# Performance work log

Measured on AMD Instinct MI355X. Metric: run time of the kernel, lower is better.

## Reference

```python
import jax, jax.numpy as jnp
import numpy as np

EPS = 1e-6
MOMENTUM = 0.9


def _normalize(x, eps=EPS):
    # Matches torch F.normalize: x / clamp_min(||x||, eps)
    n = jnp.linalg.norm(x, axis=-1, keepdims=True)
    return x / jnp.maximum(n, eps)


def setup_inputs() -> dict:
    key = jax.random.key(0)
    k1, k2 = jax.random.split(key)
    embeddings = jax.random.normal(k1, (131072, 512), dtype=jnp.float32)
    prototypes = jax.random.normal(k2, (1024, 512), dtype=jnp.float32)
    return {"embeddings": embeddings, "prototypes": prototypes}


def reference(embeddings, prototypes):
    # Steady-state update path of PrototypeBank.update (filled == bank_size).
    K = prototypes.shape[0]
    e = _normalize(embeddings)                      # [N, D]
    active = _normalize(prototypes)                 # [K, D]
    sims = jnp.einsum('nd,kd->nk', e, active)       # [N, K]
    assign = jnp.argmax(sims, axis=1)               # [N] int
    # per-prototype masked mean via segment reduction
    sums = jax.ops.segment_sum(e, assign, num_segments=K)          # [K, D]
    counts = jax.ops.segment_sum(jnp.ones((e.shape[0],), e.dtype), assign,
                                 num_segments=K)                    # [K]
    has = counts > 0
    cluster_mean = sums / jnp.maximum(counts, 1.0)[:, None]
    # EMA uses the RAW stored prototype (not the normalized copy), then renormalizes
    updated = MOMENTUM * prototypes + (1.0 - MOMENTUM) * cluster_mean
    updated = _normalize(updated)
    new_prototypes = jnp.where(has[:, None], updated, prototypes)
    return new_prototypes
```

## Files before the change

kernel.cpp:

```cpp
#include <hip/hip_runtime.h>


#define D 512
#define NPROTO 1024
#define ROWS 64

typedef __attribute__((ext_vector_type(8))) unsigned short ushort8;
typedef __attribute__((ext_vector_type(8))) __bf16 bfrag8;
typedef __attribute__((ext_vector_type(4))) float f32x4;

static __device__ inline unsigned short f2bf(float f) {
    unsigned int u = __float_as_uint(f);
    u = u + 0x7FFFu + ((u >> 16) & 1u);
    return (unsigned short)(u >> 16);
}

__global__ __launch_bounds__(256) void norm_protos_kernel(
    const float* __restrict__ protos, unsigned short* __restrict__ pbf,
    int* __restrict__ counts)
{
    const int wave = threadIdx.x >> 6, lane = threadIdx.x & 63;
    const int row = blockIdx.x * 4 + wave;
    const float* src = protos + (size_t)row * D + lane * 8;
    float4 v0 = *(const float4*)src;
    float4 v1 = *(const float4*)(src + 4);
    float ss = v0.x*v0.x + v0.y*v0.y + v0.z*v0.z + v0.w*v0.w
             + v1.x*v1.x + v1.y*v1.y + v1.z*v1.z + v1.w*v1.w;
    #pragma unroll
    for (int off = 32; off > 0; off >>= 1) ss += __shfl_xor(ss, off, 64);
    const float inv = 1.0f / fmaxf(sqrtf(ss), 1e-6f);
    ushort8 w;
    w[0] = f2bf(v0.x*inv); w[1] = f2bf(v0.y*inv); w[2] = f2bf(v0.z*inv); w[3] = f2bf(v0.w*inv);
    w[4] = f2bf(v1.x*inv); w[5] = f2bf(v1.y*inv); w[6] = f2bf(v1.z*inv); w[7] = f2bf(v1.w*inv);
    const int g = row >> 4, cl = row & 15;
    const int ks = lane >> 2, q = lane & 3;
    *(ushort8*)(pbf + (size_t)(g * 16 + ks) * 512 + (q * 16 + cl) * 8) = w;
    if (blockIdx.x == 0) ((int4*)counts)[threadIdx.x] = (int4){0, 0, 0, 0};
}

__global__ __launch_bounds__(512, 4) void assign_kernel(
    const float* __restrict__ emb, const unsigned short* __restrict__ pbf,
    int* __restrict__ assign, float* __restrict__ invnorm, int* __restrict__ counts)
{
    __shared__ __align__(16) unsigned short eT[ROWS * D];
    const int tid = threadIdx.x;
    const int wave = tid >> 6, lane = tid & 63;
    const int rowbase = blockIdx.x * ROWS;
    const int cl = lane & 15, quad = lane >> 4;

    for (int rr = 0; rr < 8; ++rr) {
        const int rloc = wave * 8 + rr;
        const float* src = emb + (size_t)(rowbase + rloc) * D + lane * 8;
        float4 v0 = *(const float4*)src;
        float4 v1 = *(const float4*)(src + 4);
        float ss = v0.x*v0.x + v0.y*v0.y + v0.z*v0.z + v0.w*v0.w
                 + v1.x*v1.x + v1.y*v1.y + v1.z*v1.z + v1.w*v1.w;
        #pragma unroll
        for (int off = 32; off > 0; off >>= 1) ss += __shfl_xor(ss, off, 64);
        const float inv = 1.0f / fmaxf(sqrtf(ss), 1e-6f);
        if (lane == 0) invnorm[rowbase + rloc] = inv;
        ushort8 w;
        w[0] = f2bf(v0.x*inv); w[1] = f2bf(v0.y*inv); w[2] = f2bf(v0.z*inv); w[3] = f2bf(v0.w*inv);
        w[4] = f2bf(v1.x*inv); w[5] = f2bf(v1.y*inv); w[6] = f2bf(v1.z*inv); w[7] = f2bf(v1.w*inv);
        const int slot = lane ^ (rloc & 7);
        *(ushort8*)(&eT[rloc * D + slot * 8]) = w;
    }
    __syncthreads();

    float rmax[4][4];
    int   ridx[4][4];
    #pragma unroll
    for (int m = 0; m < 4; ++m)
        #pragma unroll
        for (int r = 0; r < 4; ++r) { rmax[m][r] = -3.4e38f; ridx[m][r] = 0; }

    const int colq = wave * 128;
    const unsigned short* bb = pbf + (size_t)colq * 512 + lane * 8;

    for (int ng = 0; ng < 2; ++ng) {
        const int colbase = colq + ng * 64;
        const unsigned short* bg = bb + (size_t)ng * 64 * 512;
        f32x4 acc[4][4];
        #pragma unroll
        for (int m = 0; m < 4; ++m)
            #pragma unroll
            for (int n = 0; n < 4; ++n) acc[m][n] = (f32x4){0.f, 0.f, 0.f, 0.f};

        #pragma unroll 2
        for (int ks = 0; ks < 16; ++ks) {
            bfrag8 a[4], b[4];
            #pragma unroll
            for (int m = 0; m < 4; ++m) {
                const int rloc = m * 16 + cl;
                const int slot = (ks * 4 + quad) ^ (rloc & 7);
                a[m] = *(const bfrag8*)(&eT[rloc * D + slot * 8]);
            }
            #pragma unroll
            for (int n = 0; n < 4; ++n)
                b[n] = *(const bfrag8*)(bg + n * 8192 + ks * 512);
            #pragma unroll
            for (int n = 0; n < 4; ++n)
                #pragma unroll
                for (int m = 0; m < 4; ++m)
                    acc[m][n] = __builtin_amdgcn_mfma_f32_16x16x32_bf16(a[m], b[n], acc[m][n], 0, 0, 0);
        }
        #pragma unroll
        for (int n = 0; n < 4; ++n) {
            const int idx = colbase + n * 16 + cl;
            #pragma unroll
            for (int m = 0; m < 4; ++m)
                #pragma unroll
                for (int r = 0; r < 4; ++r) {
                    const float v = acc[m][n][r];
                    if (v > rmax[m][r]) { rmax[m][r] = v; ridx[m][r] = idx; }
                }
        }
    }

    #pragma unroll
    for (int m = 0; m < 4; ++m)
        #pragma unroll
        for (int r = 0; r < 4; ++r) {
            float v = rmax[m][r]; int idx = ridx[m][r];
            #pragma unroll
            for (int off = 1; off < 16; off <<= 1) {
                const float ov = __shfl_xor(v, off, 64);
                const int   oi = __shfl_xor(idx, off, 64);
                if (ov > v || (ov == v && oi < idx)) { v = ov; idx = oi; }
            }
            rmax[m][r] = v; ridx[m][r] = idx;
        }

    __syncthreads();
    float* swmax = (float*)eT;
    int*   swidx = (int*)&eT[1024];
    if (cl == 0) {
        #pragma unroll
        for (int m = 0; m < 4; ++m)
            #pragma unroll
            for (int r = 0; r < 4; ++r) {
                const int lrow = m * 16 + quad * 4 + r;
                swmax[wave * 64 + lrow] = rmax[m][r];
                swidx[wave * 64 + lrow] = ridx[m][r];
            }
    }
    __syncthreads();
    if (tid < 64) {
        float v = swmax[tid]; int idx = swidx[tid];
        #pragma unroll
        for (int w = 1; w < 8; ++w) {
            const float ov = swmax[w * 64 + tid];
            const int   oi = swidx[w * 64 + tid];
            if (ov > v || (ov == v && oi < idx)) { v = ov; idx = oi; }
        }
        assign[rowbase + tid] = idx;
        atomicAdd(&counts[idx], 1);
    }
}

__global__ __launch_bounds__(1024) void prefix_kernel(
    const int* __restrict__ counts, int* __restrict__ offsets, int* __restrict__ cursor)
{
    __shared__ int sc[NPROTO];
    const int t = threadIdx.x;
    const int c = counts[t];
    sc[t] = c;
    __syncthreads();
    #pragma unroll
    for (int off = 1; off < NPROTO; off <<= 1) {
        const int v = (t >= off) ? sc[t - off] : 0;
        __syncthreads();
        sc[t] += v;
        __syncthreads();
    }
    const int excl = sc[t] - c;
    offsets[t] = excl;
    cursor[t]  = excl;
}

__global__ __launch_bounds__(256) void scatter_kernel(
    const int* __restrict__ assign, int* __restrict__ cursor, int* __restrict__ bin)
{
    const int i = blockIdx.x * 256 + threadIdx.x;
    const int k = assign[i];
    const int pos = atomicAdd(&cursor[k], 1);
    bin[pos] = i;
}

__global__ __launch_bounds__(256) void update_kernel(
    const float* __restrict__ emb, const float* __restrict__ protos,
    const int* __restrict__ bin, const int* __restrict__ counts,
    const int* __restrict__ offsets, const float* __restrict__ invnorm,
    float* __restrict__ out)
{
    __shared__ float red[4];
    const int k = blockIdx.x, t = threadIdx.x;
    const int cnt = counts[k], off = offsets[k];
    float acc0 = 0.f, acc1 = 0.f;

    int j = 0;
    for (; j + 4 <= cnt; j += 4) {
        const int r0 = bin[off + j],     r1 = bin[off + j + 1];
        const int r2 = bin[off + j + 2], r3 = bin[off + j + 3];
        const float s0 = invnorm[r0], s1 = invnorm[r1];
        const float s2 = invnorm[r2], s3 = invnorm[r3];
        const float2 v0 = *(const float2*)(emb + (size_t)r0 * D + 2 * t);
        const float2 v1 = *(const float2*)(emb + (size_t)r1 * D + 2 * t);
        const float2 v2 = *(const float2*)(emb + (size_t)r2 * D + 2 * t);
        const float2 v3 = *(const float2*)(emb + (size_t)r3 * D + 2 * t);
        acc0 += v0.x * s0; acc1 += v0.y * s0;
        acc0 += v1.x * s1; acc1 += v1.y * s1;
        acc0 += v2.x * s2; acc1 += v2.y * s2;
        acc0 += v3.x * s3; acc1 += v3.y * s3;
    }
    for (; j < cnt; ++j) {
        const int r = bin[off + j];
        const float s = invnorm[r];
        const float2 v = *(const float2*)(emb + (size_t)r * D + 2 * t);
        acc0 += v.x * s; acc1 += v.y * s;
    }

    const float denom = fmaxf((float)cnt, 1.0f);
    const float m0 = acc0 / denom, m1 = acc1 / denom;
    const float p0 = protos[(size_t)k * D + 2 * t];
    const float p1 = protos[(size_t)k * D + 2 * t + 1];
    const float u0 = 0.9f * p0 + 0.1f * m0;
    const float u1 = 0.9f * p1 + 0.1f * m1;
    float ss = u0 * u0 + u1 * u1;
    #pragma unroll
    for (int off2 = 32; off2 > 0; off2 >>= 1) ss += __shfl_xor(ss, off2, 64);
    if ((t & 63) == 0) red[t >> 6] = ss;
    __syncthreads();
    const float tot = red[0] + red[1] + red[2] + red[3];
    const float inv = 1.0f / fmaxf(sqrtf(tot), 1e-6f);
    out[(size_t)k * D + 2 * t]     = (cnt > 0) ? u0 * inv : p0;
    out[(size_t)k * D + 2 * t + 1] = (cnt > 0) ? u1 * inv : p1;
}

extern "C" void kernel_launch(void* const* d_in, const int* in_sizes, int n_in,
                              void* d_out, int out_size, void* d_ws, size_t ws_size,
                              hipStream_t stream)
{
    const float* emb    = (const float*)d_in[0];
    const float* protos = (const float*)d_in[1];
    float* out = (float*)d_out;
    const int n_emb = in_sizes[0] / D;

    char* ws = (char*)d_ws;
    unsigned short* pbf = (unsigned short*)ws;
    int*   assign  = (int*)  (ws + (1 << 20));
    float* invnorm = (float*)(ws + (1 << 20) + (512 << 10));
    int*   counts  = (int*)  (ws + (2 << 20));
    int*   offsets = (int*)  (ws + (2 << 20) + (4 << 10));
    int*   cursor  = (int*)  (ws + (2 << 20) + (8 << 10));
    int*   bin     = (int*)  (ws + (2 << 20) + (12 << 10));

    norm_protos_kernel<<<NPROTO / 4, 256, 0, stream>>>(protos, pbf, counts);
    assign_kernel<<<n_emb / ROWS, 512, 0, stream>>>(emb, pbf, assign, invnorm, counts);
    prefix_kernel<<<1, 1024, 0, stream>>>(counts, offsets, cursor);
    scatter_kernel<<<n_emb / 256, 256, 0, stream>>>(assign, cursor, bin);
    update_kernel<<<NPROTO, 256, 0, stream>>>(emb, protos, bin, counts, offsets, invnorm, out);
}
```

Before: 617.1 us.

## Drop per-row scaling before argmax, reduce argmax per tile, vectorize update gather

```diff
diff --git a/kernel.cpp b/kernel.cpp
--- a/kernel.cpp
+++ b/kernel.cpp
@@ -43,6 +43,8 @@
     int* __restrict__ assign, float* __restrict__ invnorm, int* __restrict__ counts)
 {
     __shared__ __align__(16) unsigned short eT[ROWS * D];
+    __shared__ float swmax[16][64];
+    __shared__ int   swidx[16][64];
     const int tid = threadIdx.x;
     const int wave = tid >> 6, lane = tid & 63;
     const int rowbase = blockIdx.x * ROWS;
@@ -57,42 +59,30 @@
                  + v1.x*v1.x + v1.y*v1.y + v1.z*v1.z + v1.w*v1.w;
         #pragma unroll
         for (int off = 32; off > 0; off >>= 1) ss += __shfl_xor(ss, off, 64);
-        const float inv = 1.0f / fmaxf(sqrtf(ss), 1e-6f);
-        if (lane == 0) invnorm[rowbase + rloc] = inv;
+        if (lane == 0) invnorm[rowbase + rloc] = 1.0f / fmaxf(sqrtf(ss), 1e-6f);
         ushort8 w;
-        w[0] = f2bf(v0.x*inv); w[1] = f2bf(v0.y*inv); w[2] = f2bf(v0.z*inv); w[3] = f2bf(v0.w*inv);
-        w[4] = f2bf(v1.x*inv); w[5] = f2bf(v1.y*inv); w[6] = f2bf(v1.z*inv); w[7] = f2bf(v1.w*inv);
+        w[0] = f2bf(v0.x); w[1] = f2bf(v0.y); w[2] = f2bf(v0.z); w[3] = f2bf(v0.w);
+        w[4] = f2bf(v1.x); w[5] = f2bf(v1.y); w[6] = f2bf(v1.z); w[7] = f2bf(v1.w);
         const int slot = lane ^ (rloc & 7);
         *(ushort8*)(&eT[rloc * D + slot * 8]) = w;
     }
     __syncthreads();
 
-    float rmax[4][4];
-    int   ridx[4][4];
-    #pragma unroll
-    for (int m = 0; m < 4; ++m)
-        #pragma unroll
-        for (int r = 0; r < 4; ++r) { rmax[m][r] = -3.4e38f; ridx[m][r] = 0; }
-
-    const int colq = wave * 128;
-    const unsigned short* bb = pbf + (size_t)colq * 512 + lane * 8;
-
     for (int ng = 0; ng < 2; ++ng) {
-        const int colbase = colq + ng * 64;
-        const unsigned short* bg = bb + (size_t)ng * 64 * 512;
+        const int colbase = wave * 128 + ng * 64;
+        const unsigned short* bg = pbf + (size_t)colbase * 512 + lane * 8;
         f32x4 acc[4][4];
         #pragma unroll
         for (int m = 0; m < 4; ++m)
             #pragma unroll
             for (int n = 0; n < 4; ++n) acc[m][n] = (f32x4){0.f, 0.f, 0.f, 0.f};
 
-        #pragma unroll 2
         for (int ks = 0; ks < 16; ++ks) {
             bfrag8 a[4], b[4];
             #pragma unroll
             for (int m = 0; m < 4; ++m) {
                 const int rloc = m * 16 + cl;
-                const int slot = (ks * 4 + quad) ^ (rloc & 7);
+                const int slot = (ks * 4 + quad) ^ (cl & 7);
                 a[m] = *(const bfrag8*)(&eT[rloc * D + slot * 8]);
             }
             #pragma unroll
@@ -104,53 +94,39 @@
                 for (int m = 0; m < 4; ++m)
                     acc[m][n] = __builtin_amdgcn_mfma_f32_16x16x32_bf16(a[m], b[n], acc[m][n], 0, 0, 0);
         }
-        #pragma unroll
-        for (int n = 0; n < 4; ++n) {
-            const int idx = colbase + n * 16 + cl;
-            #pragma unroll
-            for (int m = 0; m < 4; ++m)
+
+        #pragma unroll
+        for (int m = 0; m < 4; ++m)
+            #pragma unroll
+            for (int r = 0; r < 4; ++r) {
+                float v = acc[m][0][r];
+                int idx = colbase + cl;
                 #pragma unroll
-                for (int r = 0; r < 4; ++r) {
-                    const float v = acc[m][n][r];
-                    if (v > rmax[m][r]) { rmax[m][r] = v; ridx[m][r] = idx; }
+                for (int n = 1; n < 4; ++n) {
+                    const float c = acc[m][n][r];
+                    const int ci = colbase + n * 16 + cl;
+                    if (c > v) { v = c; idx = ci; }
                 }
-        }
-    }
-
-    #pragma unroll
-    for (int m = 0; m < 4; ++m)
-        #pragma unroll
-        for (int r = 0; r < 4; ++r) {
-            float v = rmax[m][r]; int idx = ridx[m][r];
-            #pragma unroll
-            for (int off = 1; off < 16; off <<= 1) {
-                const float ov = __shfl_xor(v, off, 64);
-                const int   oi = __shfl_xor(idx, off, 64);
-                if (ov > v || (ov == v && oi < idx)) { v = ov; idx = oi; }
+                #pragma unroll
+                for (int off = 1; off < 16; off <<= 1) {
+                    const float ov = __shfl_xor(v, off, 64);
+                    const int   oi = __shfl_xor(idx, off, 64);
+                    if (ov > v || (ov == v && oi < idx)) { v = ov; idx = oi; }
+                }
+                if (cl == 0) {
+                    swmax[wave * 2 + ng][m * 16 + quad * 4 + r] = v;
+                    swidx[wave * 2 + ng][m * 16 + quad * 4 + r] = idx;
+                }
             }
-            rmax[m][r] = v; ridx[m][r] = idx;
-        }
-
-    __syncthreads();
-    float* swmax = (float*)eT;
-    int*   swidx = (int*)&eT[1024];
-    if (cl == 0) {
-        #pragma unroll
-        for (int m = 0; m < 4; ++m)
-            #pragma unroll
-            for (int r = 0; r < 4; ++r) {
-                const int lrow = m * 16 + quad * 4 + r;
-                swmax[wave * 64 + lrow] = rmax[m][r];
-                swidx[wave * 64 + lrow] = ridx[m][r];
-            }
-    }
-    __syncthreads();
+    }
+    __syncthreads();
+
     if (tid < 64) {
-        float v = swmax[tid]; int idx = swidx[tid];
-        #pragma unroll
-        for (int w = 1; w < 8; ++w) {
-            const float ov = swmax[w * 64 + tid];
-            const int   oi = swidx[w * 64 + tid];
+        float v = swmax[0][tid]; int idx = swidx[0][tid];
+        #pragma unroll
+        for (int s = 1; s < 16; ++s) {
+            const float ov = swmax[s][tid];
+            const int   oi = swidx[s][tid];
             if (ov > v || (ov == v && oi < idx)) { v = ov; idx = oi; }
         }
         assign[rowbase + tid] = idx;
@@ -193,48 +169,67 @@
     const int* __restrict__ offsets, const float* __restrict__ invnorm,
     float* __restrict__ out)
 {
-    __shared__ float red[4];
+    __shared__ float4 part[128];
+    __shared__ float red[2];
     const int k = blockIdx.x, t = threadIdx.x;
     const int cnt = counts[k], off = offsets[k];
-    float acc0 = 0.f, acc1 = 0.f;
-
-    int j = 0;
-    for (; j + 4 <= cnt; j += 4) {
-        const int r0 = bin[off + j],     r1 = bin[off + j + 1];
-        const int r2 = bin[off + j + 2], r3 = bin[off + j + 3];
+    const int par = t >> 7, colg = (t & 127) * 4;
+    float4 acc = make_float4(0.f, 0.f, 0.f, 0.f);
+
+    int jb = 0;
+    for (; jb + 4 <= cnt; jb += 4) {
+        const int r0 = bin[off + jb + par];
+        const int r1 = bin[off + jb + 2 + par];
         const float s0 = invnorm[r0], s1 = invnorm[r1];
-        const float s2 = invnorm[r2], s3 = invnorm[r3];
-        const float2 v0 = *(const float2*)(emb + (size_t)r0 * D + 2 * t);
-        const float2 v1 = *(const float2*)(emb + (size_t)r1 * D + 2 * t);
-        const float2 v2 = *(const float2*)(emb + (size_t)r2 * D + 2 * t);
-        const float2 v3 = *(const float2*)(emb + (size_t)r3 * D + 2 * t);
-        acc0 += v0.x * s0; acc1 += v0.y * s0;
-        acc0 += v1.x * s1; acc1 += v1.y * s1;
-        acc0 += v2.x * s2; acc1 += v2.y * s2;
-        acc0 += v3.x * s3; acc1 += v3.y * s3;
-    }
-    for (; j < cnt; ++j) {
-        const int r = bin[off + j];
+        const float4 v0 = *(const float4*)(emb + (size_t)r0 * D + colg);
+        const float4 v1 = *(const float4*)(emb + (size_t)r1 * D + colg);
+        acc.x += v0.x * s0; acc.y += v0.y * s0; acc.z += v0.z * s0; acc.w += v0.w * s0;
+        acc.x += v1.x * s1; acc.y += v1.y * s1; acc.z += v1.z * s1; acc.w += v1.w * s1;
+    }
+    if (jb + 2 <= cnt) {
+        const int r = bin[off + jb + par];
         const float s = invnorm[r];
-        const float2 v = *(const float2*)(emb + (size_t)r * D + 2 * t);
-        acc0 += v.x * s; acc1 += v.y * s;
-    }
-
-    const float denom = fmaxf((float)cnt, 1.0f);
-    const float m0 = acc0 / denom, m1 = acc1 / denom;
-    const float p0 = protos[(size_t)k * D + 2 * t];
-    const float p1 = protos[(size_t)k * D + 2 * t + 1];
-    const float u0 = 0.9f * p0 + 0.1f * m0;
-    const float u1 = 0.9f * p1 + 0.1f * m1;
-    float ss = u0 * u0 + u1 * u1;
+        const float4 v = *(const float4*)(emb + (size_t)r * D + colg);
+        acc.x += v.x * s; acc.y += v.y * s; acc.z += v.z * s; acc.w += v.w * s;
+        jb += 2;
+    }
+    if (par == 0 && jb < cnt) {
+        const int r = bin[off + jb];
+        const float s = invnorm[r];
+        const float4 v = *(const float4*)(emb + (size_t)r * D + colg);
+        acc.x += v.x * s; acc.y += v.y * s; acc.z += v.z * s; acc.w += v.w * s;
+    }
+
+    if (par == 1) part[t & 127] = acc;
+    __syncthreads();
+
+    float4 u, p4;
+    float ss = 0.f;
+    if (par == 0) {
+        const float4 o = part[t];
+        acc.x += o.x; acc.y += o.y; acc.z += o.z; acc.w += o.w;
+        const float denom = fmaxf((float)cnt, 1.0f);
+        p4 = *(const float4*)(protos + (size_t)k * D + colg);
+        u.x = 0.9f * p4.x + 0.1f * acc.x / denom;
+        u.y = 0.9f * p4.y + 0.1f * acc.y / denom;
+        u.z = 0.9f * p4.z + 0.1f * acc.z / denom;
+        u.w = 0.9f * p4.w + 0.1f * acc.w / denom;
+        ss = u.x*u.x + u.y*u.y + u.z*u.z + u.w*u.w;
+    }
     #pragma unroll
-    for (int off2 = 32; off2 > 0; off2 >>= 1) ss += __shfl_xor(ss, off2, 64);
-    if ((t & 63) == 0) red[t >> 6] = ss;
-    __syncthreads();
-    const float tot = red[0] + red[1] + red[2] + red[3];
-    const float inv = 1.0f / fmaxf(sqrtf(tot), 1e-6f);
-    out[(size_t)k * D + 2 * t]     = (cnt > 0) ? u0 * inv : p0;
-    out[(size_t)k * D + 2 * t + 1] = (cnt > 0) ? u1 * inv : p1;
+    for (int o2 = 32; o2 > 0; o2 >>= 1) ss += __shfl_xor(ss, o2, 64);
+    if ((t & 63) == 0 && par == 0) red[t >> 6] = ss;
+    __syncthreads();
+    if (par == 0) {
+        const float tot = red[0] + red[1];
+        const float inv = 1.0f / fmaxf(sqrtf(tot), 1e-6f);
+        float4 o;
+        o.x = (cnt > 0) ? u.x * inv : p4.x;
+        o.y = (cnt > 0) ? u.y * inv : p4.y;
+        o.z = (cnt > 0) ? u.z * inv : p4.z;
+        o.w = (cnt > 0) ? u.w * inv : p4.w;
+        *(float4*)(out + (size_t)k * D + colg) = o;
+    }
 }
 
 extern "C" void kernel_launch(void* const* d_in, const int* in_sizes, int n_in,
```

Result: slower. 1.148 ms (+86.0%).
